# Optimization experiments

Hardware: AMD Instinct MI355X
Metric: run time of the kernel (lower is better)

Reference implementation:

```python
import jax, jax.numpy as jnp
import numpy as np

NUM_HEADS = 4

def _pos_encoding(seq_len, d, dtype):
    # standard sinusoidal positional encoding [seq_len, d]
    pos = jnp.arange(seq_len, dtype=jnp.float32)[:, None]
    i = jnp.arange(0, d, 2, dtype=jnp.float32)
    div = jnp.exp(-jnp.log(10000.0) * i / d)
    ang = pos * div
    pe = jnp.zeros((seq_len, d), jnp.float32)
    pe = pe.at[:, 0::2].set(jnp.sin(ang)).at[:, 1::2].set(jnp.cos(ang))
    return pe.astype(dtype)

def _layer_norm(x, g, b, eps=1e-5):
    m = jnp.mean(x, axis=-1, keepdims=True)
    v = jnp.mean(jnp.square(x - m), axis=-1, keepdims=True)
    return (x - m) / jnp.sqrt(v + eps) * g + b

def setup_inputs() -> dict:
    key = jax.random.key(0)
    ks = jax.random.split(key, 10)
    B, S, H, W, N = 8, 512, 768, 8, 4096
    s = 0.02
    token_reps = jax.random.normal(ks[0], (B, S, H), jnp.float32)
    starts = jax.random.randint(ks[1], (B, N), 0, S - W)
    widths = jax.random.randint(ks[2], (B, N), 1, W + 1)
    span_ids = jnp.stack([starts, starts + widths], axis=-1)  # end > start, end <= S
    span_masks = jax.random.randint(ks[3], (B, N), 0, 2)
    return dict(
        token_reps=token_reps,
        dummy_query=jax.random.normal(ks[4], (H,), jnp.float32) * s,
        in_proj_w=jax.random.normal(ks[5], (3 * H, H), jnp.float32) * s,
        in_proj_b=jnp.zeros((3 * H,), jnp.float32),
        out_w=jax.random.normal(ks[6], (H, H), jnp.float32) * s,
        out_b=jnp.zeros((H,), jnp.float32),
        ln_g=jnp.ones((H,), jnp.float32),
        ln_b=jnp.zeros((H,), jnp.float32),
        ffn_w1=jax.random.normal(ks[7], (H, 4 * H), jnp.float32) * s,
        ffn_b1=jnp.zeros((4 * H,), jnp.float32),
        ffn_w2=jax.random.normal(ks[8], (4 * H, H), jnp.float32) * s,
        ffn_b2=jnp.zeros((H,), jnp.float32),
        span_ids=span_ids,
        span_masks=span_masks,
    )

def reference(token_reps, dummy_query, in_proj_w, in_proj_b, out_w, out_b,
              ln_g, ln_b, ffn_w1, ffn_b1, ffn_w2, ffn_b2, span_ids, span_masks):
    B, S, H = token_reps.shape
    N = span_ids.shape[1]
    NH = NUM_HEADS
    DH = H // NH
    # sequence positional encoding (dropout is identity in eval mode)
    x = token_reps + _pos_encoding(S, H, token_reps.dtype)[None]
    Wq, Wk, Wv = jnp.split(in_proj_w, 3, axis=0)
    bq, bk, bv = jnp.split(in_proj_b, 3)
    # single shared dummy query -> per-head query [NH, DH]
    q = (dummy_query @ Wq.T + bq).reshape(NH, DH)
    k = (x @ Wk.T + bk).reshape(B, S, NH, DH)
    v = (x @ Wv.T + bv).reshape(B, S, NH, DH)
    # scores are identical across spans since the query is shared: [B, NH, S]
    scores = jnp.einsum('hd,bshd->bhs', q, k) / jnp.sqrt(jnp.asarray(DH, x.dtype))
    pos = jnp.arange(S)
    # per-span key validity: start <= pos < end, and span not masked out  [B, N, S]
    valid = (pos[None, None, :] >= span_ids[..., 0:1]) & \
            (pos[None, None, :] < span_ids[..., 1:2]) & \
            (span_masks[..., None] != 0)
    logits = jnp.where(valid[:, :, None, :], scores[:, None, :, :], -1e9)  # [B,N,NH,S]
    w = jax.nn.softmax(logits, axis=-1)
    attn = jnp.einsum('bnhs,bshd->bnhd', w, v).reshape(B, N, H)
    attn = attn @ out_w.T + out_b
    h1 = _layer_norm(attn + dummy_query, ln_g, ln_b)
    ffn = jax.nn.relu(h1 @ ffn_w1 + ffn_b1) @ ffn_w2 + ffn_b2
    out = _layer_norm(ffn + h1, ln_g, ln_b)
    # masked spans produce exact zeros, matching the original loop
    return out * (span_masks[..., None] != 0).astype(out.dtype)
```

## Files before the change

### kernel.cpp

```cpp
#include <hip/hip_runtime.h>
#include <hip/hip_bf16.h>

#define Bb 8
#define Ss 512
#define Hh 768
#define NHh 4
#define Nn 4096
#define ROWS (Bb * Nn)
#define SCB 128

typedef _Float16 f16x8 __attribute__((ext_vector_type(8)));
typedef _Float16 f16x4 __attribute__((ext_vector_type(4)));
typedef _Float16 f16x2 __attribute__((ext_vector_type(2)));
typedef float f32x4 __attribute__((ext_vector_type(4)));

#define DEVINL __device__ __forceinline__

DEVINL void gld_lds16(const void* g, void* l) {
  __builtin_amdgcn_global_load_lds(
      (const __attribute__((address_space(1))) void*)g,
      (__attribute__((address_space(3))) void*)l, 16, 0, 0);
}

DEVINL float block_sum256(float v, float* red) {
#pragma unroll
  for (int o = 32; o; o >>= 1) v += __shfl_xor(v, o, 64);
  const int wid = threadIdx.x >> 6, lane = threadIdx.x & 63;
  if (lane == 0) red[wid] = v;
  __syncthreads();
  float r = red[0] + red[1] + red[2] + red[3];
  __syncthreads();
  return r;
}

__global__ __launch_bounds__(256) void x_kernel(const float* __restrict__ tok,
                                                _Float16* __restrict__ x) {
  int idx = blockIdx.x * 256 + threadIdx.x;
  int t = idx % 384;
  int bs = idx / 384;
  int s = bs & (Ss - 1);
  float div = expf(-(float)t * 0.02398526138535465f);
  float ang = (float)s * div;
  float sv = sinf(ang), cv = cosf(ang);
  const float2 tv = ((const float2*)tok)[(size_t)bs * 384 + t];
  f16x2 o;
  o[0] = (_Float16)(tv.x + sv);
  o[1] = (_Float16)(tv.y + cv);
  *(f16x2*)&x[(size_t)bs * Hh + 2 * t] = o;
}

__global__ __launch_bounds__(256) void q_kernel(const float* __restrict__ dq,
                                                const float* __restrict__ ipw,
                                                const float* __restrict__ ipb,
                                                float* __restrict__ qout) {
  __shared__ float red[4];
  int o = blockIdx.x;
  const float* wr = ipw + (size_t)o * Hh;
  float s = 0.f;
#pragma unroll
  for (int e = 0; e < 3; e++) {
    int j = threadIdx.x + 256 * e;
    s += dq[j] * wr[j];
  }
  s = block_sum256(s, red);
  if (threadIdx.x == 0) qout[o] = s + ipb[o];
}

__global__ __launch_bounds__(256) void c_kernel(const float* __restrict__ q,
                                                const float* __restrict__ ipw,
                                                const float* __restrict__ ipb,
                                                float* __restrict__ cout,
                                                float* __restrict__ sbias) {
  __shared__ float red[4];
  int bid = blockIdx.x;
  int t = threadIdx.x;
  if (bid < 3072) {
    int h = bid / Hh;
    int j = bid - h * Hh;
    float s = 0.f;
    if (t < 192) s = q[h * 192 + t] * ipw[(size_t)(Hh + h * 192 + t) * Hh + j];
    s = block_sum256(s, red);
    if (t == 0) cout[bid] = s;
  } else {
    int h = bid - 3072;
    float s = 0.f;
    if (t < 192) s = q[h * 192 + t] * ipb[Hh + h * 192 + t];
    s = block_sum256(s, red);
    if (t == 0) sbias[h] = s;
  }
}

__global__ __launch_bounds__(256) void score_kernel(
    const _Float16* __restrict__ x, const float* __restrict__ c,
    const float* __restrict__ sbias, float* __restrict__ scores) {
  int bs = blockIdx.x;
  int wid = threadIdx.x >> 6, lane = threadIdx.x & 63;
  const _Float16* xr = x + (size_t)bs * Hh;
  const float* ch = c + wid * Hh;
  float s = 0.f;
#pragma unroll
  for (int e = 0; e < 12; e++) {
    int j = e * 64 + lane;
    s += (float)xr[j] * ch[j];
  }
#pragma unroll
  for (int o = 32; o; o >>= 1) s += __shfl_xor(s, o, 64);
  if (lane == 0) {
    int b = bs >> 9, pos = bs & (Ss - 1);
    scores[((size_t)(b * NHh + wid)) * Ss + pos] =
        (s + sbias[wid]) * 0.07216878364870322f;
  }
}

__global__ __launch_bounds__(256) void cvt_kernel(const float* __restrict__ in,
                                                  _Float16* __restrict__ out) {
  int i = blockIdx.x * 256 + threadIdx.x;
  float4 f = ((const float4*)in)[i];
  f16x4 o;
  o[0] = (_Float16)f.x;
  o[1] = (_Float16)f.y;
  o[2] = (_Float16)f.z;
  o[3] = (_Float16)f.w;
  ((f16x4*)out)[i] = o;
}

__global__ __launch_bounds__(256) void trcvt_kernel(const float* __restrict__ in,
                                                    _Float16* __restrict__ out,
                                                    int R, int C) {
  __shared__ float tile[32][33];
  int c0 = blockIdx.x * 32, r0 = blockIdx.y * 32;
  int tx = threadIdx.x & 31, ty0 = threadIdx.x >> 5;
#pragma unroll
  for (int ty = ty0; ty < 32; ty += 8)
    tile[ty][tx] = in[(size_t)(r0 + ty) * C + c0 + tx];
  __syncthreads();
#pragma unroll
  for (int ty = ty0; ty < 32; ty += 8)
    out[(size_t)(c0 + ty) * R + r0 + tx] = (_Float16)tile[tx][ty];
}

__global__ __launch_bounds__(256) void scan1_kernel(const int* __restrict__ mask,
                                                    int* __restrict__ bsum) {
  int r = blockIdx.x * 256 + threadIdx.x;
  unsigned long long b = __ballot(mask[r] != 0);
  __shared__ int wsum[4];
  int lane = threadIdx.x & 63, wid = threadIdx.x >> 6;
  if (lane == 0) wsum[wid] = __popcll(b);
  __syncthreads();
  if (threadIdx.x == 0)
    bsum[blockIdx.x] = wsum[0] + wsum[1] + wsum[2] + wsum[3];
}
__global__ __launch_bounds__(64) void scan2_kernel(const int* __restrict__ bsum,
                                                   int* __restrict__ boff,
                                                   int* __restrict__ cnt) {
  if (threadIdx.x == 0) {
    int acc = 0;
    for (int i = 0; i < SCB; i++) {
      boff[i] = acc;
      acc += bsum[i];
    }
    *cnt = acc;
  }
}
__global__ __launch_bounds__(256) void cidx_kernel(const int* __restrict__ mask,
                                                   const int* __restrict__ boff,
                                                   int* __restrict__ cidx) {
  int r = blockIdx.x * 256 + threadIdx.x;
  int m = mask[r] != 0;
  unsigned long long b = __ballot(m);
  __shared__ int wsum[4];
  int lane = threadIdx.x & 63, wid = threadIdx.x >> 6;
  if (lane == 0) wsum[wid] = __popcll(b);
  __syncthreads();
  int pre = 0;
#pragma unroll
  for (int i = 0; i < 3; i++)
    if (i < wid) pre += wsum[i];
  pre += __popcll(b & ((1ULL << lane) - 1));
  if (m) cidx[r] = boff[blockIdx.x] + pre;
}

template <int RELU, int BN>
__global__ __launch_bounds__(256, 2) void gemm_nt(
    const _Float16* __restrict__ A, const _Float16* __restrict__ W,
    const float* __restrict__ bias, _Float16* __restrict__ C, int N, int K,
    const int* __restrict__ mcount) {
  const long m0 = (long)blockIdx.x * 128;
  if (mcount && m0 >= (long)*mcount) return;
  __shared__ __align__(16) _Float16 As[2][128 * 32];
  __shared__ __align__(16) _Float16 Bs[2][BN * 32];
  const int tid = threadIdx.x;
  const int wid = tid >> 6;
  const int lane = tid & 63;
  const long n0 = (long)blockIdx.y * BN;

  const int c0 = wid * 64 + lane;
  const int c1 = c0 + 256;
  const int sw0 = ((c0 & 3) ^ ((c0 >> 3) & 3)) * 8;
  const int sw1 = ((c1 & 3) ^ ((c1 >> 3) & 3)) * 8;
  const _Float16* gA0 = A + (m0 + (c0 >> 2)) * K + sw0;
  const _Float16* gA1 = A + (m0 + (c1 >> 2)) * K + sw1;
  const _Float16* gB0 = W + (n0 + (c0 >> 2)) * K + sw0;
  const _Float16* gB1 = W + (n0 + (c1 >> 2)) * K + sw1;

  const int wr = (wid >> 1) * 64;
  const int wc = (wid & 1) * (BN / 2);
  constexpr int NF = BN / 32;
  const int fr = lane & 15;
  const int fkb = lane >> 4;

  f32x4 acc[4][NF];
#pragma unroll
  for (int mi = 0; mi < 4; mi++)
#pragma unroll
    for (int ni = 0; ni < NF; ni++) acc[mi][ni] = (f32x4){0.f, 0.f, 0.f, 0.f};

#define STAGE(buf, k0)                                                  \
  do {                                                                  \
    gld_lds16(gA0 + (k0), &As[buf][wid * 512]);                         \
    gld_lds16(gA1 + (k0), &As[buf][2048 + wid * 512]);                  \
    gld_lds16(gB0 + (k0), &Bs[buf][wid * 512]);                         \
    if constexpr (BN == 128) gld_lds16(gB1 + (k0), &Bs[buf][2048 + wid * 512]); \
  } while (0)

#define COMPUTE(buf)                                                          \
  do {                                                                        \
    f16x8 af[4], bf[NF];                                                      \
    _Pragma("unroll") for (int i = 0; i < 4; i++) {                           \
      int r_ = wr + i * 16 + fr;                                              \
      af[i] = *(const f16x8*)&As[buf][r_ * 32 + ((fkb ^ ((r_ >> 1) & 3)) * 8)]; \
    }                                                                         \
    _Pragma("unroll") for (int i = 0; i < NF; i++) {                          \
      int r_ = wc + i * 16 + fr;                                              \
      bf[i] = *(const f16x8*)&Bs[buf][r_ * 32 + ((fkb ^ ((r_ >> 1) & 3)) * 8)]; \
    }                                                                         \
    _Pragma("unroll") for (int mi = 0; mi < 4; mi++)                          \
        _Pragma("unroll") for (int ni = 0; ni < NF; ni++)                     \
            acc[mi][ni] = __builtin_amdgcn_mfma_f32_16x16x32_f16(             \
                af[mi], bf[ni], acc[mi][ni], 0, 0, 0);                        \
  } while (0)

  const int nt = K >> 5;
  STAGE(0, 0);
  __syncthreads();
  int t = 0;
  for (; t + 2 < nt; t += 2) {
    STAGE(1, (t + 1) * 32);
    COMPUTE(0);
    __syncthreads();
    STAGE(0, (t + 2) * 32);
    COMPUTE(1);
    __syncthreads();
  }
  STAGE(1, (t + 1) * 32);
  COMPUTE(0);
  __syncthreads();
  COMPUTE(1);
#undef STAGE
#undef COMPUTE

  const int crow = (lane >> 4) * 4;
  const int ccol = lane & 15;
  float bv[NF];
#pragma unroll
  for (int ni = 0; ni < NF; ni++)
    bv[ni] = bias ? bias[n0 + wc + ni * 16 + ccol] : 0.f;
#pragma unroll
  for (int mi = 0; mi < 4; mi++)
#pragma unroll
    for (int ni = 0; ni < NF; ni++)
#pragma unroll
      for (int i = 0; i < 4; i++) {
        float v = acc[mi][ni][i] + bv[ni];
        if (RELU) v = fmaxf(v, 0.f);
        C[(m0 + wr + mi * 16 + crow + i) * (long)N + (n0 + wc + ni * 16 + ccol)] =
            (_Float16)v;
      }
}

__global__ __launch_bounds__(256) void pool_kernel(
    const _Float16* __restrict__ v, const float* __restrict__ scores,
    const int* __restrict__ span_ids, const int* __restrict__ span_masks,
    _Float16* __restrict__ attn, const int* __restrict__ cidx) {
  int r = blockIdx.x;
  if (span_masks[r] == 0) return;
  int slot = cidx[r];
  int wid = threadIdx.x >> 6, lane = threadIdx.x & 63;
  _Float16* outr = attn + (size_t)slot * Hh;
  int b = r >> 12;
  int st = span_ids[2 * r], en = span_ids[2 * r + 1];
  int wdt = en - st;
  const float* sc = scores + ((size_t)(b * NHh + wid)) * Ss + st;
  float w[8];
  float mx = -1e30f;
#pragma unroll
  for (int j = 0; j < 8; j++) {
    float t = (j < wdt) ? sc[j] : -1e30f;
    w[j] = t;
    mx = fmaxf(mx, t);
  }
  float sum = 0.f;
#pragma unroll
  for (int j = 0; j < 8; j++) {
    float e = (j < wdt) ? expf(w[j] - mx) : 0.f;
    w[j] = e;
    sum += e;
  }
  float inv = 1.f / sum;
  float a0 = 0.f, a1 = 0.f, a2 = 0.f;
#pragma unroll
  for (int j = 0; j < 8; j++) {
    if (j < wdt) {
      const _Float16* vr =
          v + ((size_t)(b * Ss + st + j)) * Hh + wid * 192 + lane;
      float wj = w[j] * inv;
      a0 += wj * (float)vr[0];
      a1 += wj * (float)vr[64];
      a2 += wj * (float)vr[128];
    }
  }
  outr[wid * 192 + lane] = (_Float16)a0;
  outr[wid * 192 + 64 + lane] = (_Float16)a1;
  outr[wid * 192 + 128 + lane] = (_Float16)a2;
}

__global__ __launch_bounds__(256) void ln0_kernel(
    _Float16* __restrict__ X, const float* __restrict__ AddV,
    const float* __restrict__ g, const float* __restrict__ bta,
    const int* __restrict__ mcount) {
  __shared__ float red[4];
  int r = blockIdx.x;
  if (r >= *mcount) return;
  int t = threadIdx.x;
  float xv[3];
#pragma unroll
  for (int e = 0; e < 3; e++) {
    int d = t + 256 * e;
    xv[e] = (float)X[(size_t)r * Hh + d] + AddV[d];
  }
  float s = xv[0] + xv[1] + xv[2];
  s = block_sum256(s, red);
  float mean = s * (1.f / 768.f);
  float vs = 0.f;
#pragma unroll
  for (int e = 0; e < 3; e++) {
    float d = xv[e] - mean;
    vs += d * d;
  }
  vs = block_sum256(vs, red);
  float inv = rsqrtf(vs * (1.f / 768.f) + 1e-5f);
#pragma unroll
  for (int e = 0; e < 3; e++) {
    int d = t + 256 * e;
    X[(size_t)r * Hh + d] = (_Float16)((xv[e] - mean) * inv * g[d] + bta[d]);
  }
}

__global__ __launch_bounds__(256) void ln1_kernel(
    const _Float16* __restrict__ F2c, const _Float16* __restrict__ h1c,
    const int* __restrict__ cidx, const float* __restrict__ g,
    const float* __restrict__ bta, const int* __restrict__ mask,
    float* __restrict__ out) {
  __shared__ float red[4];
  int r = blockIdx.x;
  int t = threadIdx.x;
  float* orow = out + (size_t)r * Hh;
  if (mask[r] == 0) {
#pragma unroll
    for (int e = 0; e < 3; e++) orow[t + 256 * e] = 0.f;
    return;
  }
  int c = cidx[r];
  float xv[3];
#pragma unroll
  for (int e = 0; e < 3; e++) {
    int d = t + 256 * e;
    xv[e] = (float)F2c[(size_t)c * Hh + d] + (float)h1c[(size_t)c * Hh + d];
  }
  float s = xv[0] + xv[1] + xv[2];
  s = block_sum256(s, red);
  float mean = s * (1.f / 768.f);
  float vs = 0.f;
#pragma unroll
  for (int e = 0; e < 3; e++) {
    float d = xv[e] - mean;
    vs += d * d;
  }
  vs = block_sum256(vs, red);
  float inv = rsqrtf(vs * (1.f / 768.f) + 1e-5f);
#pragma unroll
  for (int e = 0; e < 3; e++) {
    int d = t + 256 * e;
    orow[d] = (xv[e] - mean) * inv * g[d] + bta[d];
  }
}

extern "C" void kernel_launch(void* const* d_in, const int* in_sizes, int n_in,
                              void* d_out, int out_size, void* d_ws,
                              size_t ws_size, hipStream_t stream) {
  (void)out_size;
  if (n_in != 14) return;
  if (in_sizes[0] != 3145728 || in_sizes[2] != 1769472 ||
      in_sizes[3] != 2304 || in_sizes[4] != 589824 ||
      in_sizes[8] != 2359296 || in_sizes[9] != 3072 ||
      in_sizes[12] != 65536 || in_sizes[13] != 32768)
    return;

  const float* tok   = (const float*)d_in[0];
  const float* dq    = (const float*)d_in[1];
  const float* ipw   = (const float*)d_in[2];
  const float* ipb   = (const float*)d_in[3];
  const float* outw  = (const float*)d_in[4];
  const float* outb  = (const float*)d_in[5];
  const float* lng   = (const float*)d_in[6];
  const float* lnb   = (const float*)d_in[7];
  const float* w1    = (const float*)d_in[8];
  const float* b1    = (const float*)d_in[9];
  const float* w2    = (const float*)d_in[10];
  const float* b2    = (const float*)d_in[11];
  const int* spid    = (const int*)d_in[12];
  const int* spmask  = (const int*)d_in[13];

  char* ws = (char*)d_ws;
  size_t off = 0;
  auto alloc = [&](size_t bytes) {
    size_t r = off;
    off = (off + bytes + 255) & ~(size_t)255;
    return r;
  };
  _Float16* X16  = (_Float16*)(ws + alloc((size_t)Bb * Ss * Hh * 2));
  float* SC      = (float*)(ws + alloc((size_t)Bb * NHh * Ss * 4));
  float* Q       = (float*)(ws + alloc(768 * 4));
  float* Cc      = (float*)(ws + alloc(3072 * 4));
  float* SB      = (float*)(ws + alloc(4 * 4));
  _Float16* WV16 = (_Float16*)(ws + alloc((size_t)768 * 768 * 2));
  _Float16* OW16 = (_Float16*)(ws + alloc((size_t)768 * 768 * 2));
  _Float16* WT1  = (_Float16*)(ws + alloc((size_t)3072 * 768 * 2));
  _Float16* WT2  = (_Float16*)(ws + alloc((size_t)768 * 3072 * 2));
  _Float16* ATTN = (_Float16*)(ws + alloc((size_t)ROWS * Hh * 2));
  _Float16* PROJ = (_Float16*)(ws + alloc((size_t)ROWS * Hh * 2));
  _Float16* F1   = (_Float16*)(ws + alloc((size_t)ROWS * 3072 * 2));
  if (ws_size < off) return;
  _Float16* F2 = ATTN;

  int* CIDX = (int*)X16;
  int* BSUM = (int*)X16 + ROWS;
  int* BOFF = (int*)X16 + ROWS + SCB;
  int* CNT  = (int*)X16 + ROWS + 2 * SCB;

  _Float16* V16 = (_Float16*)d_out;

  cvt_kernel<<<576, 256, 0, stream>>>(ipw + (size_t)1536 * 768, WV16);
  cvt_kernel<<<576, 256, 0, stream>>>(outw, OW16);
  trcvt_kernel<<<dim3(96, 24), 256, 0, stream>>>(w1, WT1, 768, 3072);
  trcvt_kernel<<<dim3(24, 96), 256, 0, stream>>>(w2, WT2, 3072, 768);

  x_kernel<<<(Bb * Ss * 384) / 256, 256, 0, stream>>>(tok, X16);
  q_kernel<<<768, 256, 0, stream>>>(dq, ipw, ipb, Q);
  c_kernel<<<3076, 256, 0, stream>>>(Q, ipw, ipb, Cc, SB);
  score_kernel<<<Bb * Ss, 256, 0, stream>>>(X16, Cc, SB, SC);
  gemm_nt<0, 64><<<dim3(32, 12), 256, 0, stream>>>(X16, WV16, ipb + 1536, V16,
                                                   768, 768, nullptr);
  scan1_kernel<<<SCB, 256, 0, stream>>>(spmask, BSUM);
  scan2_kernel<<<1, 64, 0, stream>>>(BSUM, BOFF, CNT);
  cidx_kernel<<<SCB, 256, 0, stream>>>(spmask, BOFF, CIDX);
  pool_kernel<<<ROWS, 256, 0, stream>>>(V16, SC, spid, spmask, ATTN, CIDX);
  gemm_nt<0, 128><<<dim3(ROWS / 128, 6), 256, 0, stream>>>(ATTN, OW16, outb,
                                                           PROJ, 768, 768, CNT);
  ln0_kernel<<<ROWS, 256, 0, stream>>>(PROJ, dq, lng, lnb, CNT);
  gemm_nt<1, 128><<<dim3(ROWS / 128, 24), 256, 0, stream>>>(PROJ, WT1, b1, F1,
                                                            3072, 768, CNT);
  gemm_nt<0, 128><<<dim3(ROWS / 128, 6), 256, 0, stream>>>(F1, WT2, b2, F2,
                                                           768, 3072, CNT);
  ln1_kernel<<<ROWS, 256, 0, stream>>>(F2, PROJ, CIDX, lng, lnb, spmask,
                                       (float*)d_out);
}
```

Baseline: 438.6 us.

## Triple-buffer GEMM LDS staging with explicit vmcnt waits and raw barriers

Moves the f16 MFMA GEMM from double to triple buffering in LDS, with two tiles in flight ahead of compute. `__syncthreads` is replaced by partial `s_waitcnt vmcnt` counts (sized to loads per stage) plus raw `s_barrier`, so global-to-LDS loads overlap more compute. The cost is 1.5x the LDS per block. The loop and tail assume the K-tile count is a multiple of three, which holds for K=768 and K=3072.

```diff
diff --git a/kernel.cpp b/kernel.cpp
--- a/kernel.cpp
+++ b/kernel.cpp
@@ -20,6 +20,15 @@
   __builtin_amdgcn_global_load_lds(
       (const __attribute__((address_space(1))) void*)g,
       (__attribute__((address_space(3))) void*)l, 16, 0, 0);
+}
+
+template <int V>
+DEVINL void wait_vmcnt() {
+  if constexpr (V == 0) asm volatile("s_waitcnt vmcnt(0)" ::: "memory");
+  else if constexpr (V == 3) asm volatile("s_waitcnt vmcnt(3)" ::: "memory");
+  else if constexpr (V == 4) asm volatile("s_waitcnt vmcnt(4)" ::: "memory");
+  else if constexpr (V == 6) asm volatile("s_waitcnt vmcnt(6)" ::: "memory");
+  else if constexpr (V == 8) asm volatile("s_waitcnt vmcnt(8)" ::: "memory");
 }
 
 DEVINL float block_sum256(float v, float* red) {
@@ -187,12 +196,13 @@
     const int* __restrict__ mcount) {
   const long m0 = (long)blockIdx.x * 128;
   if (mcount && m0 >= (long)*mcount) return;
-  __shared__ __align__(16) _Float16 As[2][128 * 32];
-  __shared__ __align__(16) _Float16 Bs[2][BN * 32];
+  __shared__ __align__(16) _Float16 As[3][128 * 32];
+  __shared__ __align__(16) _Float16 Bs[3][BN * 32];
   const int tid = threadIdx.x;
   const int wid = tid >> 6;
   const int lane = tid & 63;
   const long n0 = (long)blockIdx.y * BN;
+  constexpr int LPS = (BN == 128) ? 4 : 3;
 
   const int c0 = wid * 64 + lane;
   const int c1 = c0 + 256;
@@ -240,24 +250,37 @@
                 af[mi], bf[ni], acc[mi][ni], 0, 0, 0);                        \
   } while (0)
 
+#define ITER_RESTAGE(b, knext)              \
+  do {                                      \
+    wait_vmcnt<2 * LPS>();                  \
+    __builtin_amdgcn_s_barrier();           \
+    COMPUTE(b);                             \
+    __builtin_amdgcn_s_barrier();           \
+    STAGE(b, (knext));                      \
+  } while (0)
+
   const int nt = K >> 5;
   STAGE(0, 0);
-  __syncthreads();
+  STAGE(1, 32);
+  STAGE(2, 64);
   int t = 0;
-  for (; t + 2 < nt; t += 2) {
-    STAGE(1, (t + 1) * 32);
-    COMPUTE(0);
-    __syncthreads();
-    STAGE(0, (t + 2) * 32);
-    COMPUTE(1);
-    __syncthreads();
-  }
-  STAGE(1, (t + 1) * 32);
+  for (; t <= nt - 6; t += 3) {
+    ITER_RESTAGE(0, (t + 3) * 32);
+    ITER_RESTAGE(1, (t + 4) * 32);
+    ITER_RESTAGE(2, (t + 5) * 32);
+  }
+  wait_vmcnt<2 * LPS>();
+  __builtin_amdgcn_s_barrier();
   COMPUTE(0);
-  __syncthreads();
+  wait_vmcnt<LPS>();
+  __builtin_amdgcn_s_barrier();
   COMPUTE(1);
+  wait_vmcnt<0>();
+  __builtin_amdgcn_s_barrier();
+  COMPUTE(2);
 #undef STAGE
 #undef COMPUTE
+#undef ITER_RESTAGE
 
   const int crow = (lane >> 4) * 4;
   const int ccol = lane & 15;
```

After: 403.8 us. 1.09x faster.
